# Kernel tuning notes

Measured on AMD Instinct MI355X. Metric: run time of the kernel, lower is better.

## Reference

```python
import jax, jax.numpy as jnp
import numpy as np

RATIO = 1.0 / 32  # spacial_ratio
HOUT = 7          # pooled_h
WOUT = 7          # pooled_w
S = 2             # sub_bin_size = int(sqrt(n_sampled=4))


def setup_inputs() -> dict:
    key = jax.random.key(0)
    k1, k2, k3, k4, k5, k6 = jax.random.split(key, 6)
    B, C, H, W = 4, 256, 50, 50
    N = 1024
    img_w, img_h = W / RATIO, H / RATIO
    features = jax.random.normal(k1, (B, C, H, W), dtype=jnp.float32)
    b = jax.random.randint(k2, (N,), 0, B).astype(jnp.float32)
    x1 = jax.random.uniform(k3, (N,), minval=0.0, maxval=img_w - 232.0)
    y1 = jax.random.uniform(k4, (N,), minval=0.0, maxval=img_h - 232.0)
    bw = jax.random.uniform(k5, (N,), minval=32.0, maxval=232.0)
    bh = jax.random.uniform(k6, (N,), minval=32.0, maxval=232.0)
    rois = jnp.stack([b, x1, y1, x1 + bw, y1 + bh], axis=1)  # [N, 5]
    return {"features": features, "rois": rois}


def _roi_align(features, rois):
    B, C, H, W = features.shape
    fW = jnp.float32(W)
    fH = jnp.float32(H)
    b_idx = rois[:, 0].astype(jnp.int32)            # [N]
    box = rois[:, 1:] * RATIO                       # [N, 4] in feature coords
    bx1 = jnp.clip(box[:, 0], 0.0, fW)
    by1 = jnp.clip(box[:, 1], 0.0, fH)
    bx2 = jnp.clip(box[:, 2], 0.0, fW)
    by2 = jnp.clip(box[:, 3], 0.0, fH)
    roi_valid = (bx2 - bx1 > 0) & (by2 - by1 > 0)   # [N]
    bin_w = (bx2 - bx1) / WOUT                      # [N]
    bin_h = (by2 - by1) / HOUT

    jj = jnp.arange(WOUT, dtype=jnp.float32)
    ii = jnp.arange(HOUT, dtype=jnp.float32)
    # bin edges; y2/x2 computed from the UNclamped start, then clamped (matches original order)
    x1u = bx1[:, None] + jj * bin_w[:, None]        # [N, WOUT]
    x2b = jnp.clip(x1u + bin_w[:, None], 0.0, fW)
    x1b = jnp.clip(x1u, 0.0, fW)
    y1u = by1[:, None] + ii * bin_h[:, None]        # [N, HOUT]
    y2b = jnp.clip(y1u + bin_h[:, None], 0.0, fH)
    y1b = jnp.clip(y1u, 0.0, fH)
    bin_valid = (y2b > y1b)[:, :, None] & (x2b > x1b)[:, None, :]  # [N, HOUT, WOUT]

    # SxS sample-point centers inside each bin (sub_bin = bin / S, center offset 0.5)
    cc = jnp.arange(S, dtype=jnp.float32) + 0.5
    px = x1b[:, :, None] + cc * (bin_w / S)[:, None, None]  # [N, WOUT, S]
    py = y1b[:, :, None] + cc * (bin_h / S)[:, None, None]  # [N, HOUT, S]

    xl = jnp.clip(jnp.floor(px), 0, W - 1).astype(jnp.int32)
    xh = jnp.clip(xl + 1, 0, W - 1)
    yl = jnp.clip(jnp.floor(py), 0, H - 1).astype(jnp.int32)
    yh = jnp.clip(yl + 1, 0, H - 1)
    wxh = px - xl  # (x - x1)
    wxl = xh - px  # (x2 - x)
    wyb = py - yl  # (y - y1)
    wyt = yh - py  # (y2 - y)

    feats = features.transpose(0, 2, 3, 1)          # [B, H, W, C]
    bI = b_idx[:, None, None, None, None]           # [N,1,1,1,1]
    # x varies over (WOUT, sx) -> broadcast axes (2,4); y over (HOUT, sy) -> axes (1,3)
    XL = xl[:, None, :, None, :]
    XH = xh[:, None, :, None, :]
    YL = yl[:, :, None, :, None]
    YH = yh[:, :, None, :, None]
    WXh = wxh[:, None, :, None, :, None]
    WXl = wxl[:, None, :, None, :, None]
    WYb = wyb[:, :, None, :, None, None]
    WYt = wyt[:, :, None, :, None, None]

    v_tl = feats[bI, YL, XL]   # [N, HOUT, WOUT, S, S, C]
    v_tr = feats[bI, YL, XH]
    v_bl = feats[bI, YH, XL]
    v_br = feats[bI, YH, XH]
    top = WXh * v_tr + WXl * v_tl
    bot = WXh * v_br + WXl * v_bl
    val = WYb * bot + WYt * top                     # [N, HOUT, WOUT, S, S, C]

    pooled = val.max(axis=(3, 4))                   # max over sample grid -> [N, HOUT, WOUT, C]
    mask = bin_valid & roi_valid[:, None, None]
    pooled = jnp.where(mask[..., None], pooled, 0.0)
    return pooled.transpose(0, 3, 1, 2)             # [N, C, HOUT, WOUT]


def reference(features, rois):
    return _roi_align(features, rois)
```

## Files before the change

kernel.cpp:

```cpp
#include <hip/hip_runtime.h>


namespace {

constexpr int B_ = 4, C_ = 256, H_ = 50, W_ = 50;
constexpr int HW = H_ * W_;
constexpr int HO = 7, WO = 7, NBIN = HO * WO;
constexpr int CH = 128;
constexpr int OUT_PER_ROI = C_ * NBIN;
constexpr int OUT_HALF = CH * NBIN;
constexpr int LD = 129;
constexpr float RATIO = 1.0f / 32.0f;

__global__ __launch_bounds__(256) void transpose_tiled(
    const float* __restrict__ f, float* __restrict__ ft)
{
    __shared__ float tile[64][65];
    const int bt   = blockIdx.x;
    const int hw_t = bt % 40;
    const int c_t  = (bt / 40) % 4;
    const int b    = bt / 160;
    const int hw0 = hw_t * 64, c0 = c_t * 64;
    const int lx = threadIdx.x & 63;
    const int ly = threadIdx.x >> 6;

#pragma unroll
    for (int k = 0; k < 16; ++k) {
        const int c  = c0 + k * 4 + ly;
        const int hw = hw0 + lx;
        if (hw < HW)
            tile[k * 4 + ly][lx] = f[((size_t)b * C_ + c) * HW + hw];
    }
    __syncthreads();
#pragma unroll
    for (int k = 0; k < 16; ++k) {
        const int hw = hw0 + k * 4 + ly;
        if (hw < HW)
            ft[((size_t)b * HW + hw) * C_ + c0 + lx] = tile[lx][k * 4 + ly];
    }
}

template<int AX, int AY>
__device__ __forceinline__ float2 bin_max2(const float2 p[3][3],
                                           const float4 wa, const float4 wb)
{
    float2 s[2][2];
#pragma unroll
    for (int sy = 0; sy < 2; ++sy) {
#pragma unroll
        for (int sx = 0; sx < 2; ++sx) {
            const int xk = AX * sx, yj = AY * sy;
            const float wxh = sx ? wa.y : wa.x;
            const float wxl = sx ? wa.w : wa.z;
            const float wyb = sy ? wb.y : wb.x;
            const float wyt = sy ? wb.w : wb.z;
            const float2 tl = p[yj][xk],     tr = p[yj][xk + 1];
            const float2 bl = p[yj + 1][xk], br = p[yj + 1][xk + 1];
            float2 o;
            o.x = wyb * (wxh * br.x + wxl * bl.x) + wyt * (wxh * tr.x + wxl * tl.x);
            o.y = wyb * (wxh * br.y + wxl * bl.y) + wyt * (wxh * tr.y + wxl * tl.y);
            s[sy][sx] = o;
        }
    }
    float2 m;
    m.x = fmaxf(fmaxf(s[0][0].x, s[0][1].x), fmaxf(s[1][0].x, s[1][1].x));
    m.y = fmaxf(fmaxf(s[0][0].y, s[0][1].y), fmaxf(s[1][0].y, s[1][1].y));
    return m;
}

__global__ __launch_bounds__(256, 5) void roialign_main(
    const float* __restrict__ ft,
    const float* __restrict__ rois,
    float* __restrict__ out)
{
    __shared__ float stage[NBIN * LD];
    __shared__ __align__(16) float    wts[NBIN][8];
    __shared__ __align__(16) unsigned offp[NBIN][12];

    const int bid  = blockIdx.x;
    const int n    = bid >> 1;
    const int half = bid & 1;
    const int tid  = threadIdx.x;
    const int wave = tid >> 6;
    const int lane = tid & 63;
    const float fW = (float)W_, fH = (float)H_;

    if (tid < NBIN) {
        const int ii = tid / WO, jj = tid % WO;
        const float* r = rois + n * 5;
        const float bx1 = fminf(fmaxf(r[1] * RATIO, 0.0f), fW);
        const float by1 = fminf(fmaxf(r[2] * RATIO, 0.0f), fH);
        const float bx2 = fminf(fmaxf(r[3] * RATIO, 0.0f), fW);
        const float by2 = fminf(fmaxf(r[4] * RATIO, 0.0f), fH);
        const bool roi_valid = (bx2 - bx1 > 0.0f) && (by2 - by1 > 0.0f);
        const float bin_w = (bx2 - bx1) * (1.0f / (float)WO);
        const float bin_h = (by2 - by1) * (1.0f / (float)HO);

        const float x1u = bx1 + (float)jj * bin_w;
        const float x1b = fminf(fmaxf(x1u, 0.0f), fW);
        const float x2b = fminf(fmaxf(x1u + bin_w, 0.0f), fW);
        const float y1u = by1 + (float)ii * bin_h;
        const float y1b = fminf(fmaxf(y1u, 0.0f), fH);
        const float y2b = fminf(fmaxf(y1u + bin_h, 0.0f), fH);
        const float vf = (roi_valid && (y2b > y1b) && (x2b > x1b)) ? 1.0f : 0.0f;

        int xl[2], yl[2];
#pragma unroll
        for (int s = 0; s < 2; ++s) {
            const float px = x1b + ((float)s + 0.5f) * (bin_w * 0.5f);
            int l = (int)floorf(px);
            l = min(max(l, 0), W_ - 1);
            const int h = min(l + 1, W_ - 1);
            xl[s] = l;
            wts[tid][0 + s] = vf * (px - (float)l);
            wts[tid][2 + s] = vf * ((float)h - px);

            const float py = y1b + ((float)s + 0.5f) * (bin_h * 0.5f);
            int t = (int)floorf(py);
            t = min(max(t, 0), H_ - 1);
            const int u = min(t + 1, H_ - 1);
            yl[s] = t;
            wts[tid][4 + s] = py - (float)t;
            wts[tid][6 + s] = (float)u - py;
        }
        const int X0 = xl[0], Y0 = yl[0];
        const int ax = min(xl[1] - X0, 1);
        const int ay = min(yl[1] - Y0, 1);
        const int pxs0 = X0, pxs1 = min(X0 + 1, W_ - 1), pxs2 = min(X0 + 2, W_ - 1);
        const int pys0 = Y0, pys1 = min(Y0 + 1, H_ - 1), pys2 = min(Y0 + 2, H_ - 1);
        const int px_[3] = {pxs0, pxs1, pxs2};
        const int py_[3] = {pys0, pys1, pys2};
#pragma unroll
        for (int j = 0; j < 3; ++j)
#pragma unroll
            for (int k = 0; k < 3; ++k)
                offp[tid][j * 3 + k] = (unsigned)(py_[j] * W_ + px_[k]);
        offp[tid][9]  = (unsigned)(ax | (ay << 1));
        offp[tid][10] = 0u;
        offp[tid][11] = 0u;
    }
    __syncthreads();

    int b = (int)rois[n * 5];
    b = min(max(b, 0), B_ - 1);
    const float2* pb = (const float2*)(ft + (size_t)b * HW * C_ + half * CH) + lane;

    const int s0 = (wave * NBIN) >> 2;
    const int e0 = ((wave + 1) * NBIN) >> 2;
    for (int bin = s0; bin < e0; ++bin) {
        const float4 wa = *(const float4*)wts[bin];
        const float4 wb = *(const float4*)(wts[bin] + 4);
        const uint4 o0 = *(const uint4*)&offp[bin][0];
        const uint4 o1 = *(const uint4*)&offp[bin][4];
        const uint2 o2 = *(const uint2*)&offp[bin][8];

        float2 p[3][3];
        p[0][0] = pb[(int)o0.x << 7];
        p[0][1] = pb[(int)o0.y << 7];
        p[0][2] = pb[(int)o0.z << 7];
        p[1][0] = pb[(int)o0.w << 7];
        p[1][1] = pb[(int)o1.x << 7];
        p[1][2] = pb[(int)o1.y << 7];
        p[2][0] = pb[(int)o1.z << 7];
        p[2][1] = pb[(int)o1.w << 7];
        p[2][2] = pb[(int)o2.x << 7];

        float2 m;
        switch (o2.y) {
            case 0u:  m = bin_max2<0, 0>(p, wa, wb); break;
            case 1u:  m = bin_max2<1, 0>(p, wa, wb); break;
            case 2u:  m = bin_max2<0, 1>(p, wa, wb); break;
            default:  m = bin_max2<1, 1>(p, wa, wb); break;
        }

        stage[bin * LD + 2 * lane]     = m.x;
        stage[bin * LD + 2 * lane + 1] = m.y;
    }
    __syncthreads();

    float* outn = out + (size_t)n * OUT_PER_ROI + (size_t)half * OUT_HALF;
    for (int k = tid; k < OUT_HALF; k += 256) {
        const int ch  = k / NBIN;
        const int bin = k - ch * NBIN;
        outn[k] = stage[bin * LD + ch];
    }
}

}

extern "C" void kernel_launch(void* const* d_in, const int* in_sizes, int n_in,
                              void* d_out, int out_size, void* d_ws, size_t ws_size,
                              hipStream_t stream)
{
    const float* feats = (const float*)d_in[0];
    const float* rois  = (const float*)d_in[1];
    float* out = (float*)d_out;
    const int N = in_sizes[1] / 5;
    float* ft = (float*)d_ws;

    hipLaunchKernelGGL(transpose_tiled, dim3(B_ * 4 * 40), dim3(256), 0, stream,
                       feats, ft);
    hipLaunchKernelGGL(roialign_main, dim3(N * 2), dim3(256), 0, stream,
                       ft, rois, out);
}
```

Baseline: 107.9 us.

## Stage a 9x9 feature patch per ROI in shared memory before bilinear sampling

Each block now cooperatively loads a 9x9 spatial patch of the transposed features, covering the ROI's sample footprint, into shared memory once. All bilinear taps then read from LDS using precomputed byte offsets, which replaces the per-bin 3x3 global gathers and the templated switch over sample spacing. Blocks grow to 512 threads (8 waves), and the results are held in registers and written to a reused shared buffer for the coalesced output transpose. The aim is to cut redundant global/L2 traffic and gather latency. In exchange the block uses about 41KB of LDS and adds an extra barrier, which may lower the number of resident blocks per CU.

```diff
diff --git a/kernel.cpp b/kernel.cpp
--- a/kernel.cpp
+++ b/kernel.cpp
@@ -9,7 +9,10 @@
 constexpr int CH = 128;
 constexpr int OUT_PER_ROI = C_ * NBIN;
 constexpr int OUT_HALF = CH * NBIN;
-constexpr int LD = 129;
+constexpr int PW = 9, PH = 9;
+constexpr int NPOS = PW * PH;
+constexpr int PLD = CH;
+constexpr int SLD = 130;
 constexpr float RATIO = 1.0f / 32.0f;
 
 __global__ __launch_bounds__(256) void transpose_tiled(
@@ -40,42 +43,28 @@
     }
 }
 
-template<int AX, int AY>
-__device__ __forceinline__ float2 bin_max2(const float2 p[3][3],
-                                           const float4 wa, const float4 wb)
-{
-    float2 s[2][2];
-#pragma unroll
-    for (int sy = 0; sy < 2; ++sy) {
-#pragma unroll
-        for (int sx = 0; sx < 2; ++sx) {
-            const int xk = AX * sx, yj = AY * sy;
-            const float wxh = sx ? wa.y : wa.x;
-            const float wxl = sx ? wa.w : wa.z;
-            const float wyb = sy ? wb.y : wb.x;
-            const float wyt = sy ? wb.w : wb.z;
-            const float2 tl = p[yj][xk],     tr = p[yj][xk + 1];
-            const float2 bl = p[yj + 1][xk], br = p[yj + 1][xk + 1];
-            float2 o;
-            o.x = wyb * (wxh * br.x + wxl * bl.x) + wyt * (wxh * tr.x + wxl * tl.x);
-            o.y = wyb * (wxh * br.y + wxl * bl.y) + wyt * (wxh * tr.y + wxl * tl.y);
-            s[sy][sx] = o;
-        }
-    }
-    float2 m;
-    m.x = fmaxf(fmaxf(s[0][0].x, s[0][1].x), fmaxf(s[1][0].x, s[1][1].x));
-    m.y = fmaxf(fmaxf(s[0][0].y, s[0][1].y), fmaxf(s[1][0].y, s[1][1].y));
-    return m;
-}
-
-__global__ __launch_bounds__(256, 5) void roialign_main(
+__device__ __forceinline__ float2 bilin2(const char* pbase, const uint4 o,
+                                         const float wxh, const float wxl,
+                                         const float wyb, const float wyt)
+{
+    const float2 tl = *(const float2*)(pbase + o.x);
+    const float2 tr = *(const float2*)(pbase + o.y);
+    const float2 bl = *(const float2*)(pbase + o.z);
+    const float2 br = *(const float2*)(pbase + o.w);
+    float2 s;
+    s.x = wyb * (wxh * br.x + wxl * bl.x) + wyt * (wxh * tr.x + wxl * tl.x);
+    s.y = wyb * (wxh * br.y + wxl * bl.y) + wyt * (wxh * tr.y + wxl * tl.y);
+    return s;
+}
+
+__global__ __launch_bounds__(512) void roialign_main(
     const float* __restrict__ ft,
     const float* __restrict__ rois,
     float* __restrict__ out)
 {
-    __shared__ float stage[NBIN * LD];
+    __shared__ float smem[NPOS * PLD];
     __shared__ __align__(16) float    wts[NBIN][8];
-    __shared__ __align__(16) unsigned offp[NBIN][12];
+    __shared__ __align__(16) unsigned offp[NBIN][16];
 
     const int bid  = blockIdx.x;
     const int n    = bid >> 1;
@@ -85,16 +74,36 @@
     const int lane = tid & 63;
     const float fW = (float)W_, fH = (float)H_;
 
+    const float* r = rois + n * 5;
+    const float bx1 = fminf(fmaxf(r[1] * RATIO, 0.0f), fW);
+    const float by1 = fminf(fmaxf(r[2] * RATIO, 0.0f), fH);
+    const float bx2 = fminf(fmaxf(r[3] * RATIO, 0.0f), fW);
+    const float by2 = fminf(fmaxf(r[4] * RATIO, 0.0f), fH);
+    const float bin_w = (bx2 - bx1) * (1.0f / (float)WO);
+    const float bin_h = (by2 - by1) * (1.0f / (float)HO);
+    const float px00 = bx1 + 0.5f * (bin_w * 0.5f);
+    const float py00 = by1 + 0.5f * (bin_h * 0.5f);
+    int X0 = (int)floorf(px00); X0 = min(max(X0, 0), W_ - 1);
+    int Y0 = (int)floorf(py00); Y0 = min(max(Y0, 0), H_ - 1);
+    int b = (int)r[0];
+    b = min(max(b, 0), B_ - 1);
+
+    {
+        const int xv = min(PW, W_ - X0);
+        const int yv = min(PH, H_ - Y0);
+        const float2* pb =
+            (const float2*)(ft + ((size_t)b * HW) * C_ + half * CH) + lane;
+        for (int pos = wave; pos < NPOS; pos += 8) {
+            const int pr = pos / PW, pc = pos - pr * PW;
+            if (pr < yv && pc < xv)
+                *(float2*)&smem[pos * PLD + 2 * lane] =
+                    pb[(size_t)((Y0 + pr) * W_ + (X0 + pc)) * (C_ / 2)];
+        }
+    }
+
     if (tid < NBIN) {
         const int ii = tid / WO, jj = tid % WO;
-        const float* r = rois + n * 5;
-        const float bx1 = fminf(fmaxf(r[1] * RATIO, 0.0f), fW);
-        const float by1 = fminf(fmaxf(r[2] * RATIO, 0.0f), fH);
-        const float bx2 = fminf(fmaxf(r[3] * RATIO, 0.0f), fW);
-        const float by2 = fminf(fmaxf(r[4] * RATIO, 0.0f), fH);
         const bool roi_valid = (bx2 - bx1 > 0.0f) && (by2 - by1 > 0.0f);
-        const float bin_w = (bx2 - bx1) * (1.0f / (float)WO);
-        const float bin_h = (by2 - by1) * (1.0f / (float)HO);
 
         const float x1u = bx1 + (float)jj * bin_w;
         const float x1b = fminf(fmaxf(x1u, 0.0f), fW);
@@ -104,85 +113,76 @@
         const float y2b = fminf(fmaxf(y1u + bin_h, 0.0f), fH);
         const float vf = (roi_valid && (y2b > y1b) && (x2b > x1b)) ? 1.0f : 0.0f;
 
-        int xl[2], yl[2];
+        int xlo[2], xhi[2], ylo[2], yhi[2];
 #pragma unroll
         for (int s = 0; s < 2; ++s) {
             const float px = x1b + ((float)s + 0.5f) * (bin_w * 0.5f);
             int l = (int)floorf(px);
             l = min(max(l, 0), W_ - 1);
             const int h = min(l + 1, W_ - 1);
-            xl[s] = l;
             wts[tid][0 + s] = vf * (px - (float)l);
             wts[tid][2 + s] = vf * ((float)h - px);
-
+            xlo[s] = min(max(l - X0, 0), PW - 1);
+            xhi[s] = min(max(h - X0, 0), PW - 1);
             const float py = y1b + ((float)s + 0.5f) * (bin_h * 0.5f);
             int t = (int)floorf(py);
             t = min(max(t, 0), H_ - 1);
             const int u = min(t + 1, H_ - 1);
-            yl[s] = t;
             wts[tid][4 + s] = py - (float)t;
             wts[tid][6 + s] = (float)u - py;
+            ylo[s] = min(max(t - Y0, 0), PH - 1);
+            yhi[s] = min(max(u - Y0, 0), PH - 1);
         }
-        const int X0 = xl[0], Y0 = yl[0];
-        const int ax = min(xl[1] - X0, 1);
-        const int ay = min(yl[1] - Y0, 1);
-        const int pxs0 = X0, pxs1 = min(X0 + 1, W_ - 1), pxs2 = min(X0 + 2, W_ - 1);
-        const int pys0 = Y0, pys1 = min(Y0 + 1, H_ - 1), pys2 = min(Y0 + 2, H_ - 1);
-        const int px_[3] = {pxs0, pxs1, pxs2};
-        const int py_[3] = {pys0, pys1, pys2};
-#pragma unroll
-        for (int j = 0; j < 3; ++j)
-#pragma unroll
-            for (int k = 0; k < 3; ++k)
-                offp[tid][j * 3 + k] = (unsigned)(py_[j] * W_ + px_[k]);
-        offp[tid][9]  = (unsigned)(ax | (ay << 1));
-        offp[tid][10] = 0u;
-        offp[tid][11] = 0u;
-    }
-    __syncthreads();
-
-    int b = (int)rois[n * 5];
-    b = min(max(b, 0), B_ - 1);
-    const float2* pb = (const float2*)(ft + (size_t)b * HW * C_ + half * CH) + lane;
-
-    const int s0 = (wave * NBIN) >> 2;
-    const int e0 = ((wave + 1) * NBIN) >> 2;
-    for (int bin = s0; bin < e0; ++bin) {
-        const float4 wa = *(const float4*)wts[bin];
-        const float4 wb = *(const float4*)(wts[bin] + 4);
-        const uint4 o0 = *(const uint4*)&offp[bin][0];
-        const uint4 o1 = *(const uint4*)&offp[bin][4];
-        const uint2 o2 = *(const uint2*)&offp[bin][8];
-
-        float2 p[3][3];
-        p[0][0] = pb[(int)o0.x << 7];
-        p[0][1] = pb[(int)o0.y << 7];
-        p[0][2] = pb[(int)o0.z << 7];
-        p[1][0] = pb[(int)o0.w << 7];
-        p[1][1] = pb[(int)o1.x << 7];
-        p[1][2] = pb[(int)o1.y << 7];
-        p[2][0] = pb[(int)o1.z << 7];
-        p[2][1] = pb[(int)o1.w << 7];
-        p[2][2] = pb[(int)o2.x << 7];
-
-        float2 m;
-        switch (o2.y) {
-            case 0u:  m = bin_max2<0, 0>(p, wa, wb); break;
-            case 1u:  m = bin_max2<1, 0>(p, wa, wb); break;
-            case 2u:  m = bin_max2<0, 1>(p, wa, wb); break;
-            default:  m = bin_max2<1, 1>(p, wa, wb); break;
+#pragma unroll
+        for (int sy = 0; sy < 2; ++sy)
+#pragma unroll
+            for (int sx = 0; sx < 2; ++sx) {
+                const int base = 4 * (2 * sy + sx);
+                offp[tid][base + 0] = (unsigned)((ylo[sy] * PW + xlo[sx]) * (PLD * 4));
+                offp[tid][base + 1] = (unsigned)((ylo[sy] * PW + xhi[sx]) * (PLD * 4));
+                offp[tid][base + 2] = (unsigned)((yhi[sy] * PW + xlo[sx]) * (PLD * 4));
+                offp[tid][base + 3] = (unsigned)((yhi[sy] * PW + xhi[sx]) * (PLD * 4));
+            }
+    }
+    __syncthreads();
+
+    const char* pbase = (const char*)smem + (size_t)(8 * lane);
+    float2 mreg[7];
+#pragma unroll
+    for (int i = 0; i < 7; ++i) {
+        const int bin = wave + 8 * i;
+        if (bin < NBIN) {
+            const float4 wa = *(const float4*)wts[bin];
+            const float4 wb = *(const float4*)(wts[bin] + 4);
+            const uint4 oA = *(const uint4*)&offp[bin][0];
+            const uint4 oB = *(const uint4*)&offp[bin][4];
+            const uint4 oC = *(const uint4*)&offp[bin][8];
+            const uint4 oD = *(const uint4*)&offp[bin][12];
+            const float2 s00 = bilin2(pbase, oA, wa.x, wa.z, wb.x, wb.z);
+            const float2 s01 = bilin2(pbase, oB, wa.y, wa.w, wb.x, wb.z);
+            const float2 s10 = bilin2(pbase, oC, wa.x, wa.z, wb.y, wb.w);
+            const float2 s11 = bilin2(pbase, oD, wa.y, wa.w, wb.y, wb.w);
+            float2 m;
+            m.x = fmaxf(fmaxf(s00.x, s01.x), fmaxf(s10.x, s11.x));
+            m.y = fmaxf(fmaxf(s00.y, s01.y), fmaxf(s10.y, s11.y));
+            mreg[i] = m;
         }
-
-        stage[bin * LD + 2 * lane]     = m.x;
-        stage[bin * LD + 2 * lane + 1] = m.y;
+    }
+    __syncthreads();
+
+#pragma unroll
+    for (int i = 0; i < 7; ++i) {
+        const int bin = wave + 8 * i;
+        if (bin < NBIN)
+            *(float2*)&smem[bin * SLD + 2 * lane] = mreg[i];
     }
     __syncthreads();
 
     float* outn = out + (size_t)n * OUT_PER_ROI + (size_t)half * OUT_HALF;
-    for (int k = tid; k < OUT_HALF; k += 256) {
+    for (int k = tid; k < OUT_HALF; k += 512) {
         const int ch  = k / NBIN;
         const int bin = k - ch * NBIN;
-        outn[k] = stage[bin * LD + ch];
+        outn[k] = smem[bin * SLD + ch];
     }
 }
 
@@ -200,6 +200,6 @@
 
     hipLaunchKernelGGL(transpose_tiled, dim3(B_ * 4 * 40), dim3(256), 0, stream,
                        feats, ft);
-    hipLaunchKernelGGL(roialign_main, dim3(N * 2), dim3(256), 0, stream,
+    hipLaunchKernelGGL(roialign_main, dim3(N * 2), dim3(512), 0, stream,
                        ft, rois, out);
 }
```

After: 137.4 us. 1.27x slower.
